# Performance work log

Hardware: AMD Instinct MI355X
Metric: run time of the kernel (lower is better)

Reference implementation:

```python
import jax, jax.numpy as jnp
import numpy as np

RATIO = 2
GROUPS = 4


def conv1x1(x, w, b):
    # x: (B,C,H,W), w: (O,C), b: (O,)
    return jnp.einsum('bchw,oc->bohw', x, w) + b[None, :, None, None]


def pixel_unshuffle(x, r):
    # out[b, c*r*r + i*r + j, h, w] = x[b, c, h*r+i, w*r+j]  (torch semantics)
    B, C, H, W = x.shape
    x = x.reshape(B, C, H // r, r, W // r, r)
    x = x.transpose(0, 1, 3, 5, 2, 4)
    return x.reshape(B, C * r * r, H // r, W // r)


def grid_sample_bilinear_border(img, grid):
    # img: (N,C,H,W); grid: (N,Ho,Wo,2), grid[...,0]=x coord, grid[...,1]=y coord in [-1,1]
    # align_corners=False, padding_mode='border' (torch: clip coord to border, then bilinear)
    N, C, H, W = img.shape
    ix = ((grid[..., 0] + 1.0) * W - 1.0) * 0.5
    iy = ((grid[..., 1] + 1.0) * H - 1.0) * 0.5
    ix = jnp.clip(ix, 0.0, W - 1.0)
    iy = jnp.clip(iy, 0.0, H - 1.0)
    x0 = jnp.floor(ix)
    y0 = jnp.floor(iy)
    wx = (ix - x0)[:, None]  # (N,1,Ho,Wo) broadcast over C
    wy = (iy - y0)[:, None]
    x0i = x0.astype(jnp.int32)
    y0i = y0.astype(jnp.int32)
    x1i = jnp.minimum(x0i + 1, W - 1)
    y1i = jnp.minimum(y0i + 1, H - 1)
    gather = jax.vmap(lambda im, yy, xx: im[:, yy, xx])  # (C,Ho,Wo) per batch
    v00 = gather(img, y0i, x0i)
    v01 = gather(img, y0i, x1i)
    v10 = gather(img, y1i, x0i)
    v11 = gather(img, y1i, x1i)
    return (v00 * (1 - wx) * (1 - wy) + v01 * wx * (1 - wy)
            + v10 * (1 - wx) * wy + v11 * wx * wy)


def setup_inputs() -> dict:
    key = jax.random.key(0)
    k1, k2, k3 = jax.random.split(key, 3)
    B, C, H, W = 16, 64, 256, 256
    c_out = 2 * (GROUPS // RATIO ** 2)  # = 2
    x = jax.random.normal(k1, (B, C, H, W), jnp.float32)
    w_off = jax.random.normal(k2, (c_out, C), jnp.float32) * 0.001
    b_off = jnp.zeros((c_out,), jnp.float32)
    w_sc = jax.random.normal(k3, (c_out, C), jnp.float32) * 0.001
    b_sc = jnp.zeros((c_out,), jnp.float32)
    return {"x": x, "w_off": w_off, "b_off": b_off, "w_sc": w_sc, "b_sc": b_sc}


def reference(x, w_off, b_off, w_sc, b_sc):
    B, Cin, H, W = x.shape  # H,W divisible by RATIO -> replicate pad is a no-op
    # forward_lp with dyScope=True
    off = conv1x1(x, w_off, b_off)
    off = jax.nn.sigmoid(conv1x1(x, w_sc, b_sc)) * 0.5 * off
    off = pixel_unshuffle(off, RATIO)            # (B, 2*GROUPS, h, w)
    h, w = off.shape[2], off.shape[3]
    # x: 'b (c grp) h w -> (b grp) c h w'
    cg = Cin // GROUPS
    xg = x.reshape(B, cg, GROUPS, H, W).transpose(0, 2, 1, 3, 4).reshape(B * GROUPS, cg, H, W)
    # offset: 'b (grp two) h w -> (b grp) h w two'
    offg = off.reshape(B, GROUPS, 2, h, w).transpose(0, 1, 3, 4, 2).reshape(B * GROUPS, h, w, 2)
    # pos: stack(meshgrid(h_coord, w_coord)) -> channel 0 = h_coord, channel 1 = w_coord
    hc = jnp.arange(h, dtype=x.dtype) + 0.5
    wc = jnp.arange(w, dtype=x.dtype) + 0.5
    pos = jnp.stack(jnp.meshgrid(hc, wc, indexing='ij'), axis=-1)[None]  # (1,h,w,2)
    norm = jnp.array([w, h], dtype=x.dtype)  # normalizer = [w, h]
    grid = 2.0 * (pos + offg) / norm - 1.0
    out = grid_sample_bilinear_border(xg, grid)  # (B*GROUPS, cg, h, w)
    out = out.reshape(B, GROUPS, cg, h, w).transpose(0, 2, 1, 3, 4).reshape(B, Cin, h, w)
    return out, offg
```

## Files before the change

### kernel.cpp

```cpp
#include <hip/hip_runtime.h>
#include <math.h>

#define BATCH 16
#define CIN   64
#define HIN   256
#define WIN   256
#define HOUT  128
#define WOUT  128
#define NPIX  (HIN * WIN)
#define NPIXO (HOUT * WOUT)
#define OUT0_SIZE ((size_t)BATCH * CIN * HOUT * WOUT)

__global__ __launch_bounds__(256) void k_fused(
    const float* __restrict__ x,
    const float* __restrict__ w_off, const float* __restrict__ b_off,
    const float* __restrict__ w_sc,  const float* __restrict__ b_sc,
    float* __restrict__ out, float* __restrict__ offg)
{
    __shared__ float  sw[256];
    __shared__ float2 soff[4][16][17];
    __shared__ float  sval[16][272];

    int t = threadIdx.x;
    sw[t] = (t < 128) ? w_off[t] : w_sc[t - 128];

    int blk  = blockIdx.x;
    int b    = blk >> 6;
    int tile = blk & 63;
    int hh0  = (tile >> 3) * 16;
    int ww0  = (tile & 7) * 16;

    int row = t >> 4, col = t & 15;
    int hh = hh0 + row, ww = ww0 + col;

    const float* xb = x + (size_t)b * CIN * NPIX + (2 * hh) * WIN + 2 * ww;

    float aA0[2][2] = {{0,0},{0,0}}, aA1[2][2] = {{0,0},{0,0}};
    float aS0[2][2] = {{0,0},{0,0}}, aS1[2][2] = {{0,0},{0,0}};

    __syncthreads();

    #pragma unroll 8
    for (int c = 0; c < CIN; ++c) {
        const float* xc = xb + (size_t)c * NPIX;
        float2 r0 = *reinterpret_cast<const float2*>(xc);
        float2 r1 = *reinterpret_cast<const float2*>(xc + WIN);
        float wo0 = sw[c], wo1 = sw[64 + c], ws0 = sw[128 + c], ws1 = sw[192 + c];
        aA0[0][0] += r0.x * wo0;  aA0[0][1] += r0.y * wo0;
        aA0[1][0] += r1.x * wo0;  aA0[1][1] += r1.y * wo0;
        aA1[0][0] += r0.x * wo1;  aA1[0][1] += r0.y * wo1;
        aA1[1][0] += r1.x * wo1;  aA1[1][1] += r1.y * wo1;
        aS0[0][0] += r0.x * ws0;  aS0[0][1] += r0.y * ws0;
        aS0[1][0] += r1.x * ws0;  aS0[1][1] += r1.y * ws0;
        aS1[0][0] += r0.x * ws1;  aS1[0][1] += r0.y * ws1;
        aS1[1][0] += r1.x * ws1;  aS1[1][1] += r1.y * ws1;
    }

    float bo0 = b_off[0], bo1 = b_off[1];
    float bs0 = b_sc[0],  bs1 = b_sc[1];

    float og[4][2];
    #pragma unroll
    for (int i = 0; i < 2; ++i) {
        #pragma unroll
        for (int j = 0; j < 2; ++j) {
            float g0 = 1.0f / (1.0f + __expf(-(aS0[i][j] + bs0)));
            float g1 = 1.0f / (1.0f + __expf(-(aS1[i][j] + bs1)));
            og[i][j]     = g0 * 0.5f * (aA0[i][j] + bo0);
            og[2 + i][j] = g1 * 0.5f * (aA1[i][j] + bo1);
        }
    }

    #pragma unroll
    for (int g = 0; g < 4; ++g) {
        float2 vv = make_float2(og[g][0], og[g][1]);
        soff[g][row][col] = vv;
        size_t oi = ((size_t)((b * 4 + g) * HOUT + hh)) * WOUT + ww;
        __builtin_nontemporal_store(__builtin_bit_cast(double, vv),
                                    reinterpret_cast<double*>(offg + 2 * oi));
    }
    __syncthreads();

    int hl = t & 15, wl = t >> 4;
    int shh = hh0 + hl, sww = ww0 + wl;
    const float* xg = x + (size_t)b * CIN * NPIX;

    int sh = t >> 4, sc = t & 15;
    float* ob = out + (((size_t)b * CIN) * HOUT + (hh0 + sh)) * WOUT + (ww0 + sc);

    for (int g = 0; g < 4; ++g) {
        float2 off = soff[g][hl][wl];
        float ix = 2.0f * ((float)shh + 0.5f + off.x) - 0.5f;
        float iy = 2.0f * ((float)sww + 0.5f + off.y) - 0.5f;
        ix = fminf(fmaxf(ix, 0.0f), (float)(WIN - 1));
        iy = fminf(fmaxf(iy, 0.0f), (float)(HIN - 1));

        float x0f = floorf(ix), y0f = floorf(iy);
        float wx = ix - x0f, wy = iy - y0f;
        int x0 = (int)x0f, y0 = (int)y0f;
        int x1 = min(x0 + 1, WIN - 1);
        int y1 = min(y0 + 1, HIN - 1);

        float w00 = (1.0f - wx) * (1.0f - wy);
        float w01 = wx * (1.0f - wy);
        float w10 = (1.0f - wx) * wy;
        float w11 = wx * wy;

        int i00 = y0 * WIN + x0, i01 = y0 * WIN + x1;
        int i10 = y1 * WIN + x0, i11 = y1 * WIN + x1;

        const float* xgc = xg + (size_t)g * NPIX;

        float v[16];
        bool fastp = ((x0 & 1) == 0) && (x1 == x0 + 1);
        if (fastp) {
            #pragma unroll
            for (int c = 0; c < 16; ++c) {
                const float* xc = xgc + (size_t)c * 4 * NPIX;
                float2 a = *reinterpret_cast<const float2*>(xc + i00);
                float2 d = *reinterpret_cast<const float2*>(xc + i10);
                v[c] = a.x * w00 + a.y * w01 + d.x * w10 + d.y * w11;
            }
        } else {
            #pragma unroll
            for (int c = 0; c < 16; ++c) {
                const float* xc = xgc + (size_t)c * 4 * NPIX;
                v[c] = xc[i00] * w00 + xc[i01] * w01
                     + xc[i10] * w10 + xc[i11] * w11;
            }
        }

        __syncthreads();
        #pragma unroll
        for (int c = 0; c < 16; ++c)
            sval[c][hl * 17 + wl] = v[c];
        __syncthreads();

        #pragma unroll
        for (int c = 0; c < 16; ++c)
            __builtin_nontemporal_store(sval[c][sh * 17 + sc],
                                        &ob[(size_t)(c * 4 + g) * NPIXO]);
    }
}

extern "C" void kernel_launch(void* const* d_in, const int* in_sizes, int n_in,
                              void* d_out, int out_size, void* d_ws, size_t ws_size,
                              hipStream_t stream) {
    const float* x     = (const float*)d_in[0];
    const float* w_off = (const float*)d_in[1];
    const float* b_off = (const float*)d_in[2];
    const float* w_sc  = (const float*)d_in[3];
    const float* b_sc  = (const float*)d_in[4];

    float* out  = (float*)d_out;
    float* offg = out + OUT0_SIZE;

    k_fused<<<1024, 256, 0, stream>>>(x, w_off, b_off, w_sc, b_sc, out, offg);
}
```

Measured before the change: 97.70 us.

## Use 16-byte loads with lane-pair shuffles and vectorized output stores

Result: slower. 100.6 us (+3.0%).

```diff
diff --git a/kernel.cpp b/kernel.cpp
--- a/kernel.cpp
+++ b/kernel.cpp
@@ -11,6 +11,8 @@
 #define NPIXO (HOUT * WOUT)
 #define OUT0_SIZE ((size_t)BATCH * CIN * HOUT * WOUT)
 
+typedef __attribute__((ext_vector_type(4))) float f32x4;
+
 __global__ __launch_bounds__(256) void k_fused(
     const float* __restrict__ x,
     const float* __restrict__ w_off, const float* __restrict__ b_off,
@@ -19,7 +21,7 @@
 {
     __shared__ float  sw[256];
     __shared__ float2 soff[4][16][17];
-    __shared__ float  sval[16][272];
+    __shared__ __align__(16) float sval[5184];
 
     int t = threadIdx.x;
     sw[t] = (t < 128) ? w_off[t] : w_sc[t - 128];
@@ -32,29 +34,48 @@
 
     int row = t >> 4, col = t & 15;
     int hh = hh0 + row, ww = ww0 + col;
-
-    const float* xb = x + (size_t)b * CIN * NPIX + (2 * hh) * WIN + 2 * ww;
-
-    float aA0[2][2] = {{0,0},{0,0}}, aA1[2][2] = {{0,0},{0,0}};
-    float aS0[2][2] = {{0,0},{0,0}}, aS1[2][2] = {{0,0},{0,0}};
+    int odd = t & 1;
+    int colbase = 2 * (ww0 + (col & 14));
+
+    const float* xrow = x + (size_t)b * CIN * NPIX
+                      + (size_t)(2 * hh + odd) * WIN + colbase;
+
+    float TA0[4] = {0,0,0,0}, TA1[4] = {0,0,0,0};
+    float TS0[4] = {0,0,0,0}, TS1[4] = {0,0,0,0};
 
     __syncthreads();
 
     #pragma unroll 8
     for (int c = 0; c < CIN; ++c) {
-        const float* xc = xb + (size_t)c * NPIX;
-        float2 r0 = *reinterpret_cast<const float2*>(xc);
-        float2 r1 = *reinterpret_cast<const float2*>(xc + WIN);
+        f32x4 f = *reinterpret_cast<const f32x4*>(xrow + (size_t)c * NPIX);
         float wo0 = sw[c], wo1 = sw[64 + c], ws0 = sw[128 + c], ws1 = sw[192 + c];
-        aA0[0][0] += r0.x * wo0;  aA0[0][1] += r0.y * wo0;
-        aA0[1][0] += r1.x * wo0;  aA0[1][1] += r1.y * wo0;
-        aA1[0][0] += r0.x * wo1;  aA1[0][1] += r0.y * wo1;
-        aA1[1][0] += r1.x * wo1;  aA1[1][1] += r1.y * wo1;
-        aS0[0][0] += r0.x * ws0;  aS0[0][1] += r0.y * ws0;
-        aS0[1][0] += r1.x * ws0;  aS0[1][1] += r1.y * ws0;
-        aS1[0][0] += r0.x * ws1;  aS1[0][1] += r0.y * ws1;
-        aS1[1][0] += r1.x * ws1;  aS1[1][1] += r1.y * ws1;
-    }
+        #pragma unroll
+        for (int j = 0; j < 4; ++j) {
+            TA0[j] += f[j] * wo0;
+            TA1[j] += f[j] * wo1;
+            TS0[j] += f[j] * ws0;
+            TS1[j] += f[j] * ws1;
+        }
+    }
+
+    float rA0_0 = __shfl_xor(odd ? TA0[0] : TA0[2], 1);
+    float rA0_1 = __shfl_xor(odd ? TA0[1] : TA0[3], 1);
+    float rA1_0 = __shfl_xor(odd ? TA1[0] : TA1[2], 1);
+    float rA1_1 = __shfl_xor(odd ? TA1[1] : TA1[3], 1);
+    float rS0_0 = __shfl_xor(odd ? TS0[0] : TS0[2], 1);
+    float rS0_1 = __shfl_xor(odd ? TS0[1] : TS0[3], 1);
+    float rS1_0 = __shfl_xor(odd ? TS1[0] : TS1[2], 1);
+    float rS1_1 = __shfl_xor(odd ? TS1[1] : TS1[3], 1);
+
+    float aA0[2][2], aA1[2][2], aS0[2][2], aS1[2][2];
+    aA0[0][0] = odd ? rA0_0 : TA0[0];  aA0[0][1] = odd ? rA0_1 : TA0[1];
+    aA0[1][0] = odd ? TA0[2] : rA0_0;  aA0[1][1] = odd ? TA0[3] : rA0_1;
+    aA1[0][0] = odd ? rA1_0 : TA1[0];  aA1[0][1] = odd ? rA1_1 : TA1[1];
+    aA1[1][0] = odd ? TA1[2] : rA1_0;  aA1[1][1] = odd ? TA1[3] : rA1_1;
+    aS0[0][0] = odd ? rS0_0 : TS0[0];  aS0[0][1] = odd ? rS0_1 : TS0[1];
+    aS0[1][0] = odd ? TS0[2] : rS0_0;  aS0[1][1] = odd ? TS0[3] : rS0_1;
+    aS1[0][0] = odd ? rS1_0 : TS1[0];  aS1[0][1] = odd ? rS1_1 : TS1[1];
+    aS1[1][0] = odd ? TS1[2] : rS1_0;  aS1[1][1] = odd ? TS1[3] : rS1_1;
 
     float bo0 = b_off[0], bo1 = b_off[1];
     float bs0 = b_sc[0],  bs1 = b_sc[1];
@@ -83,11 +104,17 @@
 
     int hl = t & 15, wl = t >> 4;
     int shh = hh0 + hl, sww = ww0 + wl;
+    int oddl = t & 1;
     const float* xg = x + (size_t)b * CIN * NPIX;
 
-    int sh = t >> 4, sc = t & 15;
-    float* ob = out + (((size_t)b * CIN) * HOUT + (hh0 + sh)) * WOUT + (ww0 + sc);
-
+    int R  = (t >> 2) & 15;
+    int q  = t & 3;
+    int wv = t >> 6;
+
+    float* outb = out + (size_t)b * CIN * NPIXO
+                + (size_t)(hh0 + R) * WOUT + ww0 + q * 4;
+
+    #pragma unroll
     for (int g = 0; g < 4; ++g) {
         float2 off = soff[g][hl][wl];
         float ix = 2.0f * ((float)shh + 0.5f + off.x) - 0.5f;
@@ -106,40 +133,65 @@
         float w10 = (1.0f - wx) * wy;
         float w11 = wx * wy;
 
-        int i00 = y0 * WIN + x0, i01 = y0 * WIN + x1;
-        int i10 = y1 * WIN + x0, i11 = y1 * WIN + x1;
-
         const float* xgc = xg + (size_t)g * NPIX;
 
+        int x0p = __shfl_xor(x0, 1);
+        int y0p = __shfl_xor(y0, 1);
+        bool ok = (x1 == x0 + 1) && (y1 == y0 + 1) && (y0p == y0)
+               && (oddl ? (x0 == x0p + 2) : (x0p == x0 + 2))
+               && (((x0 - (oddl ? 2 : 0)) & 3) == 0);
+
         float v[16];
-        bool fastp = ((x0 & 1) == 0) && (x1 == x0 + 1);
-        if (fastp) {
+        if (__all(ok)) {
+            int colb = x0 - (oddl ? 2 : 0);
+            int rowL = oddl ? y1 : y0;
+            float rw0 = __shfl_xor(oddl ? w00 : w10, 1);
+            float rw1 = __shfl_xor(oddl ? w01 : w11, 1);
+            const float* basep = xgc + (size_t)rowL * WIN + colb;
             #pragma unroll
             for (int c = 0; c < 16; ++c) {
-                const float* xc = xgc + (size_t)c * 4 * NPIX;
-                float2 a = *reinterpret_cast<const float2*>(xc + i00);
-                float2 d = *reinterpret_cast<const float2*>(xc + i10);
-                v[c] = a.x * w00 + a.y * w01 + d.x * w10 + d.y * w11;
+                f32x4 f = *reinterpret_cast<const f32x4*>(basep + (size_t)c * 4 * NPIX);
+                float pOwn  = oddl ? (f[2] * w10 + f[3] * w11)
+                                   : (f[0] * w00 + f[1] * w01);
+                float pPart = oddl ? (f[0] * rw0 + f[1] * rw1)
+                                   : (f[2] * rw0 + f[3] * rw1);
+                v[c] = pOwn + __shfl_xor(pPart, 1);
             }
         } else {
-            #pragma unroll
-            for (int c = 0; c < 16; ++c) {
-                const float* xc = xgc + (size_t)c * 4 * NPIX;
-                v[c] = xc[i00] * w00 + xc[i01] * w01
-                     + xc[i10] * w10 + xc[i11] * w11;
+            int i00 = y0 * WIN + x0, i01 = y0 * WIN + x1;
+            int i10 = y1 * WIN + x0, i11 = y1 * WIN + x1;
+            bool fastp = ((x0 & 1) == 0) && (x1 == x0 + 1);
+            if (fastp) {
+                #pragma unroll
+                for (int c = 0; c < 16; ++c) {
+                    const float* xc = xgc + (size_t)c * 4 * NPIX;
+                    float2 a = *reinterpret_cast<const float2*>(xc + i00);
+                    float2 d = *reinterpret_cast<const float2*>(xc + i10);
+                    v[c] = a.x * w00 + a.y * w01 + d.x * w10 + d.y * w11;
+                }
+            } else {
+                #pragma unroll
+                for (int c = 0; c < 16; ++c) {
+                    const float* xc = xgc + (size_t)c * 4 * NPIX;
+                    v[c] = xc[i00] * w00 + xc[i01] * w01
+                         + xc[i10] * w10 + xc[i11] * w11;
+                }
             }
         }
 
         __syncthreads();
         #pragma unroll
         for (int c = 0; c < 16; ++c)
-            sval[c][hl * 17 + wl] = v[c];
+            sval[c * 324 + hl * 20 + wl] = v[c];
         __syncthreads();
 
         #pragma unroll
-        for (int c = 0; c < 16; ++c)
-            __builtin_nontemporal_store(sval[c][sh * 17 + sc],
-                                        &ob[(size_t)(c * 4 + g) * NPIXO]);
+        for (int p2 = 0; p2 < 4; ++p2) {
+            int c = wv * 4 + p2;
+            f32x4 val = *reinterpret_cast<const f32x4*>(&sval[c * 324 + R * 20 + q * 4]);
+            __builtin_nontemporal_store(val, reinterpret_cast<f32x4*>(
+                outb + (size_t)(c * 4 + g) * NPIXO));
+        }
     }
 }
 
```
